# Optimization experiments

Hardware: AMD Instinct MI355X
Metric: run time of the kernel (lower is better)

Reference implementation:

```python
import jax, jax.numpy as jnp
import numpy as np

_P = ((0, 0), (1, 1), (1, 1), (0, 0))  # pad 1 on H and W (mypadding with sigma_fill=0)

_SHAPES = [
    ("e1a", (3, 3, 3, 64)), ("e1b", (3, 3, 64, 64)),
    ("e2a", (3, 3, 64, 128)), ("e2b", (3, 3, 128, 128)),
    ("ba", (3, 3, 128, 256)), ("bb", (3, 3, 256, 256)),
    ("d2u", (3, 3, 256, 128)), ("d2a", (3, 3, 256, 128)), ("d2b", (3, 3, 128, 128)),
    ("d1u", (3, 3, 128, 64)), ("d1a", (3, 3, 128, 64)), ("d1b", (3, 3, 64, 64)),
    ("fin", (1, 1, 64, 2)),
]


def _conv(x, w):
    return jax.lax.conv_general_dilated(x, w, (1, 1), 'VALID',
                                        dimension_numbers=('NHWC', 'HWIO', 'NHWC'))


def _conv_input(x, w_mu, w_sig):
    # mu = conv(x, w_mu); sigma = (sum over patch of x^2) * softplus(w_sigma)
    mu = _conv(x, w_mu)
    ws = jax.nn.softplus(w_sig)
    k, _, cin, _ = w_mu.shape
    ones = jnp.ones((k, k, cin, 1), x.dtype)
    s = _conv(x * x, ones) * ws
    return mu, s


def _conv_inter(x, s_in, w_mu, w_sig):
    # sigma = x^2 (x) w_sig + s_in (x) w_mu^2 + s_in (x) w_sig   (patch-sum form)
    mu = _conv(x, w_mu)
    ws = jax.nn.softplus(w_sig)
    k, _, cin, _ = w_mu.shape
    ones = jnp.ones((k, k, cin, 1), x.dtype)
    s = (_conv(x * x, ones) + _conv(s_in, ones)) * ws + _conv(s_in, w_mu * w_mu)
    return mu, s


def _relu(mu, s):
    g = (mu > 0).astype(mu.dtype)  # grad of ReLU; g^2 == g
    return jnp.maximum(mu, 0.0), g * s


def _pool(mu, s):
    # 2x2/stride-2 max pool with argmax; sigma gathered at argmax locations
    B, H, W, C = mu.shape

    def win(t):
        return t.reshape(B, H // 2, 2, W // 2, 2, C).transpose(0, 1, 3, 5, 2, 4).reshape(
            B, H // 2, W // 2, C, 4)

    mw, sw = win(mu), win(s)
    idx = jnp.argmax(mw, axis=-1)[..., None]
    mu_out = jnp.take_along_axis(mw, idx, axis=-1)[..., 0]
    s_out = jnp.take_along_axis(sw, idx, axis=-1)[..., 0]
    return mu_out, s_out


def _unpool(x):
    # zero-insertion: out[b, 2i+1, 2j+1, c] = x[b, i, j, c]; shape [B, 2H+1, 2W+1, C]
    B, H, W, C = x.shape
    out = jnp.zeros((B, 2 * H + 1, 2 * W + 1, C), x.dtype)
    return out.at[:, 1::2, 1::2, :].set(x)


def _crop(enc, dec):
    dh = (enc.shape[1] - dec.shape[1]) // 2
    dw = (enc.shape[2] - dec.shape[2]) // 2
    return enc[:, dh:dh + dec.shape[1], dw:dw + dec.shape[2], :]


def _softmax_prop(mu, s):
    B, H, W, C = mu.shape
    m = mu.reshape(B, -1, C)
    sg = s.reshape(B, -1, C)
    p = jax.nn.softmax(m, axis=-1)
    eye = jnp.eye(C, dtype=p.dtype)
    grad = p[..., :, None] * eye - p[..., :, None] * p[..., None, :]  # diag(p) - p p^T
    s_out = jnp.einsum('bnij,bnj->bni', grad * grad, sg)
    return p, s_out


def setup_inputs() -> dict:
    key = jax.random.key(0)
    out = {"x": jax.random.normal(jax.random.fold_in(key, 999), (4, 128, 128, 3), dtype=jnp.float32)}
    for i, (name, sh) in enumerate(_SHAPES):
        out[f"w_mu_{name}"] = 0.1 * jax.random.normal(jax.random.fold_in(key, i), sh, dtype=jnp.float32)
        out[f"w_sig_{name}"] = jax.random.uniform(jax.random.fold_in(key, 100 + i), (sh[-1],),
                                                  minval=-12.0, maxval=-4.6, dtype=jnp.float32)
    return out


def reference(x, w_mu_e1a, w_sig_e1a, w_mu_e1b, w_sig_e1b, w_mu_e2a, w_sig_e2a,
              w_mu_e2b, w_sig_e2b, w_mu_ba, w_sig_ba, w_mu_bb, w_sig_bb,
              w_mu_d2u, w_sig_d2u, w_mu_d2a, w_sig_d2a, w_mu_d2b, w_sig_d2b,
              w_mu_d1u, w_sig_d1u, w_mu_d1a, w_sig_d1a, w_mu_d1b, w_sig_d1b,
              w_mu_fin, w_sig_fin):
    # encoder level 1
    mu, s = _conv_input(jnp.pad(x, _P), w_mu_e1a, w_sig_e1a)
    mu, s = _relu(mu, s)
    mu, s = _conv_inter(jnp.pad(mu, _P), jnp.pad(s, _P), w_mu_e1b, w_sig_e1b)
    muE1, sE1 = _relu(mu, s)                       # [4,128,128,64]
    mu, s = _pool(muE1, sE1)                       # [4,64,64,64]
    # encoder level 2
    mu, s = _conv_inter(jnp.pad(mu, _P), jnp.pad(s, _P), w_mu_e2a, w_sig_e2a)
    mu, s = _relu(mu, s)
    mu, s = _conv_inter(jnp.pad(mu, _P), jnp.pad(s, _P), w_mu_e2b, w_sig_e2b)
    muE2, sE2 = _relu(mu, s)                       # [4,64,64,128]
    mu, s = _pool(muE2, sE2)                       # [4,32,32,128]
    # bottleneck
    mu, s = _conv_inter(jnp.pad(mu, _P), jnp.pad(s, _P), w_mu_ba, w_sig_ba)
    mu, s = _relu(mu, s)
    mu, s = _conv_inter(jnp.pad(mu, _P), jnp.pad(s, _P), w_mu_bb, w_sig_bb)
    mu, s = _relu(mu, s)                           # [4,32,32,256]
    # decoder level 2
    mu, s = _unpool(mu), _unpool(s)                # [4,65,65,256]
    mu, s = _conv_inter(mu, s, w_mu_d2u, w_sig_d2u)  # VALID -> [4,63,63,128]
    mu, s = _relu(mu, s)
    mu = jnp.concatenate([mu, _crop(muE2, mu)], axis=-1)
    s = jnp.concatenate([s, _crop(sE2, s)], axis=-1)  # [4,63,63,256]
    mu, s = _conv_inter(jnp.pad(mu, _P), jnp.pad(s, _P), w_mu_d2a, w_sig_d2a)
    mu, s = _relu(mu, s)
    mu, s = _conv_inter(jnp.pad(mu, _P), jnp.pad(s, _P), w_mu_d2b, w_sig_d2b)
    mu, s = _relu(mu, s)                           # [4,63,63,128]
    # decoder level 1
    mu, s = _unpool(mu), _unpool(s)                # [4,127,127,128]
    mu, s = _conv_inter(mu, s, w_mu_d1u, w_sig_d1u)  # VALID -> [4,125,125,64]
    mu, s = _relu(mu, s)
    mu = jnp.concatenate([mu, _crop(muE1, mu)], axis=-1)
    s = jnp.concatenate([s, _crop(sE1, s)], axis=-1)  # [4,125,125,128]
    mu, s = _conv_inter(jnp.pad(mu, _P), jnp.pad(s, _P), w_mu_d1a, w_sig_d1a)
    mu, s = _relu(mu, s)
    mu, s = _conv_inter(jnp.pad(mu, _P), jnp.pad(s, _P), w_mu_d1b, w_sig_d1b)
    mu, s = _relu(mu, s)
    # 1x1 classification conv + pixel-wise softmax density propagation
    mu, s = _conv_inter(mu, s, w_mu_fin, w_sig_fin)  # [4,125,125,2]
    return _softmax_prop(mu, s)                      # ([4,15625,2], [4,15625,2])
```

## Files before the change

kernel.cpp:

```cpp
#include <hip/hip_runtime.h>
#include <math.h>


typedef __attribute__((ext_vector_type(8))) short short8;
typedef __attribute__((ext_vector_type(4))) float floatx4;

__device__ __forceinline__ float softplus_f(float x) { return log1pf(expf(x)); }

__device__ __forceinline__ unsigned short f2bf(float x) {
    unsigned int u = __float_as_uint(x);
    u = (u + 0x7FFF + ((u >> 16) & 1)) >> 16;
    return (unsigned short)u;
}
__device__ __forceinline__ float bfval(unsigned short h) {
    return __uint_as_float((unsigned int)h << 16);
}

struct WMeta {
    const float* w[12];
    const float* wsig[12];
    int woff_[12];
    int spoff_[12];
    int cin_[12];
    int cout_[12];
    int nlayers;
    int totalW;
    int totalSp;
};

__global__ void wprep_all_kernel(WMeta m,
                                 unsigned short* __restrict__ wTh,
                                 unsigned short* __restrict__ wTl,
                                 unsigned short* __restrict__ wTsq,
                                 float* __restrict__ spb)
{
    int idx = blockIdx.x * blockDim.x + threadIdx.x;
    if (idx < m.totalW) {
        int l = 0;
        while (l + 1 < m.nlayers && idx >= m.woff_[l + 1]) l++;
        int local = idx - m.woff_[l];
        int Cin = m.cin_[l], Cout = m.cout_[l];
        int per = Cin * Cout;
        int tap = local / per;
        int rem = local - tap * per;
        int co = rem / Cin;
        int ci = rem - co * Cin;
        float v = m.w[l][(size_t)(tap * Cin + ci) * Cout + co];
        unsigned short hh = f2bf(v);
        wTh[idx] = hh;
        wTl[idx] = f2bf(v - bfval(hh));
        wTsq[idx] = f2bf(v * v);
    } else if (idx < m.totalW + m.totalSp) {
        int j = idx - m.totalW;
        int l = 0;
        while (l + 1 < m.nlayers && j >= m.spoff_[l + 1]) l++;
        spb[j] = softplus_f(m.wsig[l][j - m.spoff_[l]]);
    }
}

__global__ void __launch_bounds__(256)
fused_layer_kernel(const unsigned short* __restrict__ m1h, const unsigned short* __restrict__ m1l,
                   const unsigned short* __restrict__ s1h, const unsigned short* __restrict__ s1l,
                   const unsigned short* __restrict__ m2h, const unsigned short* __restrict__ m2l,
                   const unsigned short* __restrict__ s2h, const unsigned short* __restrict__ s2l,
                   const unsigned short* __restrict__ wTh, const unsigned short* __restrict__ wTl,
                   const unsigned short* __restrict__ wTsq,
                   const float* __restrict__ spv_,
                   float* __restrict__ oMf, float* __restrict__ oSf,
                   unsigned short* __restrict__ oMh, unsigned short* __restrict__ oMl,
                   unsigned short* __restrict__ oSh, unsigned short* __restrict__ oSl,
                   int B_, int H, int W, int Hin, int Win, int unpoolMode,
                   int Cin1, int Cin2,
                   int H2, int W2, int dh, int dw, int Cout)
{
    __shared__ unsigned short ldsB[3 * 2304];
    const int tid = threadIdx.x;
    const int lane = tid & 63;
    const int wave = tid >> 6;
    const int total = B_ * H * W;
    const int Cin = Cin1 + Cin2;
    const int ntiles = Cout >> 6;
    const int nPixBlk = (total + 63) >> 6;
    const int nReal = nPixBlk * ntiles;
    const int chunk = (int)gridDim.x >> 3;
    int gid = ((int)blockIdx.x & 7) * chunk + ((int)blockIdx.x >> 3);
    if (gid >= nReal) return;
    const int coTile = gid % ntiles;
    const int pixBlk = gid / ntiles;
    const int pixBase = pixBlk * 64 + wave * 16;
    const int coBase = coTile * 64;
    const int row = lane & 15;
    const int quad = lane >> 4;

    const unsigned short* wsel0; const unsigned short* wsel1; const unsigned short* wsel2;
    int tofs0, tofs1, tofs2;
    int ldso0, ldso1, ldso2;
    {
        int u = tid * 3;
        int arr = u >> 8, rem = u & 255, co = rem >> 2, part = rem & 3;
        wsel0 = (arr == 0) ? wTh : (arr == 1) ? wTl : wTsq;
        tofs0 = co * Cin + part * 8;
        ldso0 = arr * 2304 + co * 36 + part * 8;
        u++;
        arr = u >> 8; rem = u & 255; co = rem >> 2; part = rem & 3;
        wsel1 = (arr == 0) ? wTh : (arr == 1) ? wTl : wTsq;
        tofs1 = co * Cin + part * 8;
        ldso1 = arr * 2304 + co * 36 + part * 8;
        u++;
        arr = u >> 8; rem = u & 255; co = rem >> 2; part = rem & 3;
        wsel2 = (arr == 0) ? wTh : (arr == 1) ? wTl : wTsq;
        tofs2 = co * Cin + part * 8;
        ldso2 = arr * 2304 + co * 36 + part * 8;
    }

    int P = pixBase + row;
    bool pv = P < total;
    int Pc = pv ? P : 0;
    int pb = Pc / (H * W);
    int r0i = Pc - pb * (H * W);
    int ph = r0i / W;
    int pw = r0i - ph * W;

    floatx4 accM[4], accS[4];
#pragma unroll
    for (int i = 0; i < 4; i++) {
        accM[i] = (floatx4){0.f, 0.f, 0.f, 0.f};
        accS[i] = (floatx4){0.f, 0.f, 0.f, 0.f};
    }
    const short8 zero8 = {0, 0, 0, 0, 0, 0, 0, 0};
    float qacc = 0.f;

    const size_t tapstep = (size_t)Cout * Cin;
    size_t tapbase = (size_t)coBase * Cin;

    uint4 pf0 = *(const uint4*)(wsel0 + tapbase + tofs0);
    uint4 pf1 = *(const uint4*)(wsel1 + tapbase + tofs1);
    uint4 pf2 = *(const uint4*)(wsel2 + tapbase + tofs2);

    for (int tap = 0; tap < 9; tap++, tapbase += tapstep) {
        int kh = tap / 3, kw = tap - kh * 3;
        int ih, iw;
        bool tv;
        if (unpoolMode) {
            int uh = ph + kh, uw = pw + kw;
            tv = pv && (uh & 1) && (uw & 1);
            ih = (uh - 1) >> 1;
            iw = (uw - 1) >> 1;
        } else {
            ih = ph + kh - 1;
            iw = pw + kw - 1;
            tv = pv && ((unsigned)ih < (unsigned)Hin) && ((unsigned)iw < (unsigned)Win);
        }
        if (!tv) { ih = 0; iw = 0; }
        const int nsrc = (Cin2 > 0) ? 2 : 1;
        for (int src = 0; src < nsrc; src++) {
            const int csrc = src ? Cin2 : Cin1;
            const int cofs = src ? Cin1 : 0;
            const unsigned short* aMhp = src ? m2h : m1h;
            const unsigned short* aMlp = src ? m2l : m1l;
            const unsigned short* aShp = src ? s2h : s1h;
            const unsigned short* aSlp = src ? s2l : s1l;
            size_t ab;
            if (src) ab = ((size_t)(pb * H2 + ih + dh) * W2 + (iw + dw)) * (size_t)Cin2 + quad * 8;
            else     ab = ((size_t)(pb * Hin + ih) * Win + iw) * (size_t)Cin1 + quad * 8;
            for (int kb = 0; kb < csrc; kb += 32) {
                __syncthreads();
                *(uint4*)(&ldsB[ldso0]) = pf0;
                *(uint4*)(&ldsB[ldso1]) = pf1;
                *(uint4*)(&ldsB[ldso2]) = pf2;
                __syncthreads();
                short8 aMh = zero8, aMl = zero8, aSh = zero8, aSl = zero8;
                if (tv) {
                    aMh = *(const short8*)(aMhp + ab + kb);
                    aMl = *(const short8*)(aMlp + ab + kb);
                    aSh = *(const short8*)(aShp + ab + kb);
                    aSl = *(const short8*)(aSlp + ab + kb);
#pragma unroll
                    for (int e = 0; e < 8; e++) {
                        float m = bfval((unsigned short)aMh[e]) + bfval((unsigned short)aMl[e]);
                        qacc += m * m
                              + bfval((unsigned short)aSh[e]) + bfval((unsigned short)aSl[e]);
                    }
                }
                {
                    int ncol = cofs + kb + 32;
                    size_t nbase;
                    bool hn;
                    if (ncol < Cin) { nbase = tapbase + ncol; hn = true; }
                    else            { nbase = tapbase + tapstep; hn = (tap < 8); }
                    if (hn) {
                        pf0 = *(const uint4*)(wsel0 + nbase + tofs0);
                        pf1 = *(const uint4*)(wsel1 + nbase + tofs1);
                        pf2 = *(const uint4*)(wsel2 + nbase + tofs2);
                    }
                }
#pragma unroll
                for (int nt = 0; nt < 4; nt++) {
                    int lo = (nt * 16 + row) * 36 + quad * 8;
                    short8 bh = *(const short8*)(&ldsB[lo]);
                    short8 bl = *(const short8*)(&ldsB[2304 + lo]);
                    short8 bq = *(const short8*)(&ldsB[4608 + lo]);
                    accM[nt] = __builtin_amdgcn_mfma_f32_16x16x32_bf16(aMh, bh, accM[nt], 0, 0, 0);
                    accM[nt] = __builtin_amdgcn_mfma_f32_16x16x32_bf16(aMl, bh, accM[nt], 0, 0, 0);
                    accM[nt] = __builtin_amdgcn_mfma_f32_16x16x32_bf16(aMh, bl, accM[nt], 0, 0, 0);
                    accM[nt] = __builtin_amdgcn_mfma_f32_16x16x32_bf16(aMl, bl, accM[nt], 0, 0, 0);
                    accS[nt] = __builtin_amdgcn_mfma_f32_16x16x32_bf16(aSh, bq, accS[nt], 0, 0, 0);
                    accS[nt] = __builtin_amdgcn_mfma_f32_16x16x32_bf16(aSl, bq, accS[nt], 0, 0, 0);
                }
            }
        }
    }

    qacc += __shfl_xor(qacc, 16);
    qacc += __shfl_xor(qacc, 32);

#pragma unroll
    for (int nt = 0; nt < 4; nt++) {
        int co = coBase + nt * 16 + row;
        float spv = spv_[co];
        floatx4 am = accM[nt];
        floatx4 as = accS[nt];
#pragma unroll
        for (int r = 0; r < 4; r++) {
            int P2 = pixBase + quad * 4 + r;
            float qv = __shfl(qacc, quad * 4 + r);
            if (P2 < total) {
                size_t o = (size_t)P2 * Cout + co;
                float mu = am[r];
                float s = qv * spv + as[r];
                if (!(mu > 0.f)) { mu = 0.f; s = 0.f; }
                if (oMf) oMf[o] = mu;
                if (oSf) oSf[o] = s;
                if (oMh) {
                    unsigned short mh = f2bf(mu);
                    oMh[o] = mh;
                    oMl[o] = f2bf(mu - bfval(mh));
                    unsigned short sh = f2bf(s);
                    oSh[o] = sh;
                    oSl[o] = f2bf(s - bfval(sh));
                }
            }
        }
    }
}

__global__ void conv_input_relu_kernel(const float* __restrict__ x,
                                       const float* __restrict__ w_mu,
                                       const float* __restrict__ w_sig,
                                       unsigned short* __restrict__ m_h,
                                       unsigned short* __restrict__ m_l,
                                       unsigned short* __restrict__ s_h,
                                       unsigned short* __restrict__ s_l,
                                       int B_, int H, int W, int Cin, int Cout)
{
    int co = threadIdx.x;
    int pix = blockIdx.x * blockDim.y + threadIdx.y;
    int total = B_ * H * W;
    if (pix >= total) return;
    int b = pix / (H * W);
    int rem = pix % (H * W);
    int h = rem / W, w = rem % W;

    float mu = 0.f, q = 0.f;
    for (int kh = 0; kh < 3; kh++) {
        int ih = h + kh - 1;
        if (ih < 0 || ih >= H) continue;
        for (int kw = 0; kw < 3; kw++) {
            int iw = w + kw - 1;
            if (iw < 0 || iw >= W) continue;
            const float* xp = x + ((size_t)(b * H + ih) * W + iw) * Cin;
            const float* wp = w_mu + (size_t)((kh * 3 + kw) * Cin) * Cout + co;
            for (int ci = 0; ci < Cin; ci++) {
                float xv = xp[ci];
                mu += xv * wp[(size_t)ci * Cout];
                q += xv * xv;
            }
        }
    }
    float s = q * softplus_f(w_sig[co]);
    if (!(mu > 0.f)) { mu = 0.f; s = 0.f; }
    size_t oidx = (size_t)pix * Cout + co;
    unsigned short mh = f2bf(mu);
    m_h[oidx] = mh;
    m_l[oidx] = f2bf(mu - bfval(mh));
    unsigned short sh = f2bf(s);
    s_h[oidx] = sh;
    s_l[oidx] = f2bf(s - bfval(sh));
}

__global__ void pool_kernel(const float* __restrict__ mu_in,
                            const unsigned short* __restrict__ s_h,
                            const unsigned short* __restrict__ s_l,
                            unsigned short* __restrict__ pm_h,
                            unsigned short* __restrict__ pm_l,
                            unsigned short* __restrict__ ps_h,
                            unsigned short* __restrict__ ps_l,
                            int B_, int H, int W, int C)
{
    int Ho = H / 2, Wo = W / 2;
    size_t total = (size_t)B_ * Ho * Wo * C;
    size_t idx = (size_t)blockIdx.x * blockDim.x + threadIdx.x;
    if (idx >= total) return;
    int c = idx % C;
    size_t t = idx / C;
    int w = t % Wo; t /= Wo;
    int h = t % Ho;
    int b = t / Ho;
    size_t i0 = ((size_t)(b * H + 2 * h) * W + 2 * w) * C + c;
    size_t rowStride = (size_t)W * C;
    float m00 = mu_in[i0], m01 = mu_in[i0 + C];
    float m10 = mu_in[i0 + rowStride], m11 = mu_in[i0 + rowStride + C];
    int best = 0; float bm = m00;
    if (m01 > bm) { bm = m01; best = 1; }
    if (m10 > bm) { bm = m10; best = 2; }
    if (m11 > bm) { bm = m11; best = 3; }
    size_t off = (size_t)(best >> 1) * rowStride + (size_t)(best & 1) * C;
    unsigned short mh = f2bf(bm);
    pm_h[idx] = mh;
    pm_l[idx] = f2bf(bm - bfval(mh));
    ps_h[idx] = s_h[i0 + off];
    ps_l[idx] = s_l[i0 + off];
}

__global__ void final_kernel(const float* __restrict__ mu_in,
                             const float* __restrict__ s_in,
                             const float* __restrict__ w_mu,
                             const float* __restrict__ w_sig,
                             float* __restrict__ out,
                             int B_, int H, int W, int Cin)
{
    int pix = blockIdx.x * blockDim.x + threadIdx.x;
    int total = B_ * H * W;
    if (pix >= total) return;
    const float* mp = mu_in + (size_t)pix * Cin;
    const float* sp = s_in + (size_t)pix * Cin;
    float mu0 = 0.f, mu1 = 0.f, s0a = 0.f, s1a = 0.f, q = 0.f;
    for (int ci = 0; ci < Cin; ci += 4) {
        float4 m = *(const float4*)(mp + ci);
        float4 s = *(const float4*)(sp + ci);
        float4 wa = *(const float4*)(w_mu + ci * 2);
        float4 wb = *(const float4*)(w_mu + ci * 2 + 4);
        mu0 += m.x * wa.x + m.y * wa.z + m.z * wb.x + m.w * wb.z;
        mu1 += m.x * wa.y + m.y * wa.w + m.z * wb.y + m.w * wb.w;
        s0a += s.x * (wa.x * wa.x) + s.y * (wa.z * wa.z) + s.z * (wb.x * wb.x) + s.w * (wb.z * wb.z);
        s1a += s.x * (wa.y * wa.y) + s.y * (wa.w * wa.w) + s.z * (wb.y * wb.y) + s.w * (wb.w * wb.w);
        q += m.x * m.x + s.x + m.y * m.y + s.y + m.z * m.z + s.z + m.w * m.w + s.w;
    }
    float s0 = q * softplus_f(w_sig[0]) + s0a;
    float s1 = q * softplus_f(w_sig[1]) + s1a;
    float mx = fmaxf(mu0, mu1);
    float e0 = expf(mu0 - mx), e1 = expf(mu1 - mx);
    float inv = 1.f / (e0 + e1);
    float p0 = e0 * inv, p1 = e1 * inv;
    float g00 = p0 - p0 * p0, g01 = -p0 * p1;
    float g10 = -p1 * p0,     g11 = p1 - p1 * p1;
    float so0 = g00 * g00 * s0 + g01 * g01 * s1;
    float so1 = g10 * g10 * s0 + g11 * g11 * s1;
    out[(size_t)pix * 2]     = p0;
    out[(size_t)pix * 2 + 1] = p1;
    size_t off = (size_t)total * 2;
    out[off + (size_t)pix * 2]     = so0;
    out[off + (size_t)pix * 2 + 1] = so1;
}


extern "C" void kernel_launch(void* const* d_in, const int* in_sizes, int n_in,
                              void* d_out, int out_size, void* d_ws, size_t ws_size,
                              hipStream_t stream)
{
    const float* x = (const float*)d_in[0];
    enum { E1A, E1B, E2A, E2B, BA, BB, D2U, D2A, D2B, D1U, D1A, D1B, FIN, NW };
    const float* wmu[NW];
    const float* wsig[NW];
    for (int i = 0; i < NW; i++) {
        wmu[i]  = (const float*)d_in[1 + 2 * i];
        wsig[i] = (const float*)d_in[2 + 2 * i];
    }

    const int B_ = 4;
    float* ws = (float*)d_ws;
    float* M0  = ws;
    float* SF  = ws + 4194304;
    float* spb = ws + 8519680;
    unsigned short* us = (unsigned short*)(ws + 8521728);
    const size_t NB = 4194304;
    unsigned short* aMh = us;
    unsigned short* aMl = us + NB;
    unsigned short* aSh = us + 2 * NB;
    unsigned short* aSl = us + 3 * NB;
    unsigned short* bMh = us + 4 * NB;
    unsigned short* bMl = us + 5 * NB;
    unsigned short* bSh = us + 6 * NB;
    unsigned short* bSl = us + 7 * NB;
    unsigned short* e1Mh = us + 8 * NB;
    unsigned short* e1Ml = us + 9 * NB;
    unsigned short* e1Sh = us + 10 * NB;
    unsigned short* e1Sl = us + 11 * NB;
    unsigned short* e2Mh = us + 12 * NB;
    unsigned short* e2Ml = e2Mh + 2097152;
    unsigned short* e2Sh = e2Ml + 2097152;
    unsigned short* e2Sl = e2Sh + 2097152;
    unsigned short* wTh  = e2Sl + 2097152;
    unsigned short* wTl  = wTh + 2064384;
    unsigned short* wTsq = wTl + 2064384;

    const int mlay[11]  = {E1B, E2A, E2B, BA, BB, D2U, D2A, D2B, D1U, D1A, D1B};
    const int mcin[11]  = {64, 64, 128, 128, 256, 256, 256, 128, 128, 128, 64};
    const int mcout[11] = {64, 128, 128, 256, 256, 128, 128, 128, 64, 64, 64};
    size_t woff[NW]; int spoff[NW];
    {
        WMeta meta;
        int wo = 0, so = 0;
        for (int i = 0; i < 11; i++) {
            int l = mlay[i];
            woff[l] = (size_t)wo; spoff[l] = so;
            meta.w[i] = wmu[l];
            meta.wsig[i] = wsig[l];
            meta.woff_[i] = wo;
            meta.spoff_[i] = so;
            meta.cin_[i] = mcin[i];
            meta.cout_[i] = mcout[i];
            wo += 9 * mcin[i] * mcout[i];
            so += mcout[i];
        }
        meta.nlayers = 11;
        meta.totalW = wo;
        meta.totalSp = so;
        int n = wo + so;
        wprep_all_kernel<<<dim3((n + 255) / 256), dim3(256), 0, stream>>>(
            meta, wTh, wTl, wTsq, spb);
    }

    auto flayer = [&](const unsigned short* i_mh, const unsigned short* i_ml,
                      const unsigned short* i_sh, const unsigned short* i_sl, int ci1,
                      const unsigned short* k_mh, const unsigned short* k_ml,
                      const unsigned short* k_sh, const unsigned short* k_sl,
                      int ci2, int h2, int w2, int dh, int dw,
                      int H, int W, int widx, int cout,
                      float* oMf, float* oSf,
                      unsigned short* oMh, unsigned short* oMl,
                      unsigned short* oSh, unsigned short* oSl) {
        int total = B_ * H * W;
        int nReal = ((total + 63) / 64) * (cout / 64);
        int G = ((nReal + 7) / 8) * 8;
        fused_layer_kernel<<<dim3(G), dim3(256), 0, stream>>>(
            i_mh, i_ml, i_sh, i_sl, k_mh, k_ml, k_sh, k_sl,
            wTh + woff[widx], wTl + woff[widx], wTsq + woff[widx], spb + spoff[widx],
            oMf, oSf, oMh, oMl, oSh, oSl,
            B_, H, W, H, W, 0, ci1, ci2, h2, w2, dh, dw, cout);
    };

    auto ulayer = [&](const unsigned short* i_mh, const unsigned short* i_ml,
                      const unsigned short* i_sh, const unsigned short* i_sl, int ci,
                      int Hin, int Win, int widx, int cout,
                      unsigned short* oMh, unsigned short* oMl,
                      unsigned short* oSh, unsigned short* oSl) {
        int Hout = 2 * Hin - 1, Wout = 2 * Win - 1;
        int total = B_ * Hout * Wout;
        int nReal = ((total + 63) / 64) * (cout / 64);
        int G = ((nReal + 7) / 8) * 8;
        fused_layer_kernel<<<dim3(G), dim3(256), 0, stream>>>(
            i_mh, i_ml, i_sh, i_sl, nullptr, nullptr, nullptr, nullptr,
            wTh + woff[widx], wTl + woff[widx], wTsq + woff[widx], spb + spoff[widx],
            nullptr, nullptr, oMh, oMl, oSh, oSl,
            B_, Hout, Wout, Hin, Win, 1, ci, 0, 0, 0, 0, 0, cout);
    };

    {
        int totalPix = B_ * 128 * 128;
        conv_input_relu_kernel<<<dim3((totalPix + 3) / 4), dim3(64, 4), 0, stream>>>(
            x, wmu[E1A], wsig[E1A], aMh, aMl, aSh, aSl, B_, 128, 128, 3, 64);
    }
    flayer(aMh, aMl, aSh, aSl, 64, nullptr, nullptr, nullptr, nullptr, 0, 0, 0, 0, 0,
           128, 128, E1B, 64, M0, nullptr, e1Mh, e1Ml, e1Sh, e1Sl);
    {
        size_t total = (size_t)B_ * 64 * 64 * 64;
        pool_kernel<<<dim3((total + 255) / 256), dim3(256), 0, stream>>>(
            M0, e1Sh, e1Sl, bMh, bMl, bSh, bSl, B_, 128, 128, 64);
    }
    flayer(bMh, bMl, bSh, bSl, 64, nullptr, nullptr, nullptr, nullptr, 0, 0, 0, 0, 0,
           64, 64, E2A, 128, nullptr, nullptr, aMh, aMl, aSh, aSl);
    flayer(aMh, aMl, aSh, aSl, 128, nullptr, nullptr, nullptr, nullptr, 0, 0, 0, 0, 0,
           64, 64, E2B, 128, M0, nullptr, e2Mh, e2Ml, e2Sh, e2Sl);
    {
        size_t total = (size_t)B_ * 32 * 32 * 128;
        pool_kernel<<<dim3((total + 255) / 256), dim3(256), 0, stream>>>(
            M0, e2Sh, e2Sl, bMh, bMl, bSh, bSl, B_, 64, 64, 128);
    }
    flayer(bMh, bMl, bSh, bSl, 128, nullptr, nullptr, nullptr, nullptr, 0, 0, 0, 0, 0,
           32, 32, BA, 256, nullptr, nullptr, aMh, aMl, aSh, aSl);
    flayer(aMh, aMl, aSh, aSl, 256, nullptr, nullptr, nullptr, nullptr, 0, 0, 0, 0, 0,
           32, 32, BB, 256, nullptr, nullptr, bMh, bMl, bSh, bSl);
    ulayer(bMh, bMl, bSh, bSl, 256, 32, 32, D2U, 128, aMh, aMl, aSh, aSl);
    flayer(aMh, aMl, aSh, aSl, 128, e2Mh, e2Ml, e2Sh, e2Sl, 128, 64, 64, 0, 0,
           63, 63, D2A, 128, nullptr, nullptr, bMh, bMl, bSh, bSl);
    flayer(bMh, bMl, bSh, bSl, 128, nullptr, nullptr, nullptr, nullptr, 0, 0, 0, 0, 0,
           63, 63, D2B, 128, nullptr, nullptr, aMh, aMl, aSh, aSl);
    ulayer(aMh, aMl, aSh, aSl, 128, 63, 63, D1U, 64, bMh, bMl, bSh, bSl);
    flayer(bMh, bMl, bSh, bSl, 64, e1Mh, e1Ml, e1Sh, e1Sl, 64, 128, 128, 1, 1,
           125, 125, D1A, 64, nullptr, nullptr, aMh, aMl, aSh, aSl);
    flayer(aMh, aMl, aSh, aSl, 64, nullptr, nullptr, nullptr, nullptr, 0, 0, 0, 0, 0,
           125, 125, D1B, 64, M0, SF, nullptr, nullptr, nullptr, nullptr);
    {
        int totalPix = B_ * 125 * 125;
        final_kernel<<<dim3((totalPix + 63) / 64), dim3(64), 0, stream>>>(
            M0, SF, wmu[FIN], wsig[FIN], (float*)d_out, B_, 125, 125, 64);
    }
}
```

Measured before the change: 974.2 us.

## Add parity-class unpool conv kernel that skips zero-inserted taps

Adds a dedicated kernel for the transposed-convolution (unpool + 3x3 VALID conv) layers. Output pixels are split into four parity classes, and each class iterates only over the taps that hit real (non-zero) input values: 1, 2 or 4 taps instead of 9. This removes the MFMA work and loads that the generic fused kernel spent on inserted zeros. The cost is a separate code path with more index arithmetic and scattered output stores, plus per-class tiles that can be partially empty.

```diff
diff --git a/kernel.cpp b/kernel.cpp
--- a/kernel.cpp
+++ b/kernel.cpp
@@ -244,6 +244,170 @@
     }
 }
 
+__global__ void __launch_bounds__(256)
+fused_unpool_kernel(const unsigned short* __restrict__ m1h, const unsigned short* __restrict__ m1l,
+                    const unsigned short* __restrict__ s1h, const unsigned short* __restrict__ s1l,
+                    const unsigned short* __restrict__ wTh, const unsigned short* __restrict__ wTl,
+                    const unsigned short* __restrict__ wTsq,
+                    const float* __restrict__ spv_,
+                    unsigned short* __restrict__ oMh, unsigned short* __restrict__ oMl,
+                    unsigned short* __restrict__ oSh, unsigned short* __restrict__ oSl,
+                    int B_, int H, int W, int Hin, int Win,
+                    int Cin, int Cout)
+{
+    __shared__ unsigned short ldsB[3 * 2304];
+    const int tid = threadIdx.x;
+    const int lane = tid & 63;
+    const int wave = tid >> 6;
+    const int He = (H + 1) >> 1, Hd = H >> 1;
+    const int We = (W + 1) >> 1, Wd = W >> 1;
+    const int n00 = B_ * He * We, n01 = B_ * He * Wd;
+    const int n10 = B_ * Hd * We, n11 = B_ * Hd * Wd;
+    const int nb00 = (n00 + 63) >> 6, nb01 = (n01 + 63) >> 6;
+    const int nb10 = (n10 + 63) >> 6, nb11 = (n11 + 63) >> 6;
+    const int ntiles = Cout >> 6;
+    const int nReal = (nb00 + nb01 + nb10 + nb11) * ntiles;
+    const int chunk = (int)gridDim.x >> 3;
+    int gid = ((int)blockIdx.x & 7) * chunk + ((int)blockIdx.x >> 3);
+    if (gid >= nReal) return;
+    const int coTile = gid % ntiles;
+    int bid = gid / ntiles;
+    int hpar, wpar, classN, Wc, Hc;
+    if (bid < nb00)                    { hpar = 0; wpar = 0; classN = n00; Hc = He; Wc = We; }
+    else if (bid < nb00 + nb01)        { bid -= nb00; hpar = 0; wpar = 1; classN = n01; Hc = He; Wc = Wd; }
+    else if (bid < nb00 + nb01 + nb10) { bid -= nb00 + nb01; hpar = 1; wpar = 0; classN = n10; Hc = Hd; Wc = We; }
+    else                               { bid -= nb00 + nb01 + nb10; hpar = 1; wpar = 1; classN = n11; Hc = Hd; Wc = Wd; }
+    const int coBase = coTile * 64;
+    const int row = lane & 15;
+    const int quad = lane >> 4;
+    const int pixBase = bid * 64 + wave * 16;
+
+    const unsigned short* wsel0; const unsigned short* wsel1; const unsigned short* wsel2;
+    int tofs0, tofs1, tofs2, ldso0, ldso1, ldso2;
+    {
+        int u = tid * 3;
+        int arr = u >> 8, rem = u & 255, co = rem >> 2, part = rem & 3;
+        wsel0 = (arr == 0) ? wTh : (arr == 1) ? wTl : wTsq;
+        tofs0 = co * Cin + part * 8;
+        ldso0 = arr * 2304 + co * 36 + part * 8;
+        u++;
+        arr = u >> 8; rem = u & 255; co = rem >> 2; part = rem & 3;
+        wsel1 = (arr == 0) ? wTh : (arr == 1) ? wTl : wTsq;
+        tofs1 = co * Cin + part * 8;
+        ldso1 = arr * 2304 + co * 36 + part * 8;
+        u++;
+        arr = u >> 8; rem = u & 255; co = rem >> 2; part = rem & 3;
+        wsel2 = (arr == 0) ? wTh : (arr == 1) ? wTl : wTsq;
+        tofs2 = co * Cin + part * 8;
+        ldso2 = arr * 2304 + co * 36 + part * 8;
+    }
+
+    int gp = pixBase + row;
+    bool pv = gp < classN;
+    int gpc = pv ? gp : 0;
+    int hw = Hc * Wc;
+    int img = gpc / hw;
+    int rr = gpc - img * hw;
+    int hh = ((rr / Wc) << 1) + hpar;
+    int ww = ((rr - (rr / Wc) * Wc) << 1) + wpar;
+
+    floatx4 accM[4], accS[4];
+#pragma unroll
+    for (int i = 0; i < 4; i++) {
+        accM[i] = (floatx4){0.f, 0.f, 0.f, 0.f};
+        accS[i] = (floatx4){0.f, 0.f, 0.f, 0.f};
+    }
+    const short8 zero8 = {0, 0, 0, 0, 0, 0, 0, 0};
+    float qacc = 0.f;
+
+    const size_t tapstep = (size_t)Cout * Cin;
+    const size_t cobase_off = (size_t)coBase * Cin;
+
+#pragma unroll
+    for (int a = 0; a < 2; a++) {
+        if (a == 1 && hpar == 0) break;
+        int kh = hpar ? (a << 1) : 1;
+#pragma unroll
+        for (int b = 0; b < 2; b++) {
+            if (b == 1 && wpar == 0) break;
+            int kw = wpar ? (b << 1) : 1;
+            int tap = kh * 3 + kw;
+            size_t tapbase = (size_t)tap * tapstep + cobase_off;
+            int ih = (hh + kh - 1) >> 1;
+            int iw = (ww + kw - 1) >> 1;
+            size_t ab = ((size_t)(img * Hin + ih) * Win + iw) * (size_t)Cin + quad * 8;
+            for (int kb = 0; kb < Cin; kb += 32) {
+                __syncthreads();
+                uint4 w0 = *(const uint4*)(wsel0 + tapbase + kb + tofs0);
+                uint4 w1 = *(const uint4*)(wsel1 + tapbase + kb + tofs1);
+                uint4 w2 = *(const uint4*)(wsel2 + tapbase + kb + tofs2);
+                *(uint4*)(&ldsB[ldso0]) = w0;
+                *(uint4*)(&ldsB[ldso1]) = w1;
+                *(uint4*)(&ldsB[ldso2]) = w2;
+                __syncthreads();
+                short8 aMh = zero8, aMl = zero8, aSh = zero8, aSl = zero8;
+                if (pv) {
+                    aMh = *(const short8*)(m1h + ab + kb);
+                    aMl = *(const short8*)(m1l + ab + kb);
+                    aSh = *(const short8*)(s1h + ab + kb);
+                    aSl = *(const short8*)(s1l + ab + kb);
+#pragma unroll
+                    for (int e = 0; e < 8; e++) {
+                        float m = bfval((unsigned short)aMh[e]) + bfval((unsigned short)aMl[e]);
+                        qacc += m * m
+                              + bfval((unsigned short)aSh[e]) + bfval((unsigned short)aSl[e]);
+                    }
+                }
+#pragma unroll
+                for (int nt = 0; nt < 4; nt++) {
+                    int lo = (nt * 16 + row) * 36 + quad * 8;
+                    short8 bh = *(const short8*)(&ldsB[lo]);
+                    short8 bl = *(const short8*)(&ldsB[2304 + lo]);
+                    short8 bq = *(const short8*)(&ldsB[4608 + lo]);
+                    accM[nt] = __builtin_amdgcn_mfma_f32_16x16x32_bf16(aMh, bh, accM[nt], 0, 0, 0);
+                    accM[nt] = __builtin_amdgcn_mfma_f32_16x16x32_bf16(aMl, bh, accM[nt], 0, 0, 0);
+                    accM[nt] = __builtin_amdgcn_mfma_f32_16x16x32_bf16(aMh, bl, accM[nt], 0, 0, 0);
+                    accM[nt] = __builtin_amdgcn_mfma_f32_16x16x32_bf16(aMl, bl, accM[nt], 0, 0, 0);
+                    accS[nt] = __builtin_amdgcn_mfma_f32_16x16x32_bf16(aSh, bq, accS[nt], 0, 0, 0);
+                    accS[nt] = __builtin_amdgcn_mfma_f32_16x16x32_bf16(aSl, bq, accS[nt], 0, 0, 0);
+                }
+            }
+        }
+    }
+
+    qacc += __shfl_xor(qacc, 16);
+    qacc += __shfl_xor(qacc, 32);
+
+#pragma unroll
+    for (int nt = 0; nt < 4; nt++) {
+        int co = coBase + nt * 16 + row;
+        float spv = spv_[co];
+        floatx4 am = accM[nt];
+        floatx4 as = accS[nt];
+#pragma unroll
+        for (int r = 0; r < 4; r++) {
+            int gp2 = pixBase + quad * 4 + r;
+            float qv = __shfl(qacc, quad * 4 + r);
+            if (gp2 < classN) {
+                int img2 = gp2 / hw;
+                int rr2 = gp2 - img2 * hw;
+                int h2 = ((rr2 / Wc) << 1) + hpar;
+                int w2 = ((rr2 - (rr2 / Wc) * Wc) << 1) + wpar;
+                size_t o = ((size_t)(img2 * H + h2) * W + w2) * Cout + co;
+                float mu = am[r];
+                float s = qv * spv + as[r];
+                if (!(mu > 0.f)) { mu = 0.f; s = 0.f; }
+                unsigned short mh = f2bf(mu);
+                oMh[o] = mh;
+                oMl[o] = f2bf(mu - bfval(mh));
+                unsigned short sh = f2bf(s);
+                oSh[o] = sh;
+                oSl[o] = f2bf(s - bfval(sh));
+            }
+        }
+    }
+}
+
 __global__ void conv_input_relu_kernel(const float* __restrict__ x,
                                        const float* __restrict__ w_mu,
                                        const float* __restrict__ w_sig,
@@ -456,14 +620,17 @@
                       unsigned short* oMh, unsigned short* oMl,
                       unsigned short* oSh, unsigned short* oSl) {
         int Hout = 2 * Hin - 1, Wout = 2 * Win - 1;
-        int total = B_ * Hout * Wout;
-        int nReal = ((total + 63) / 64) * (cout / 64);
+        int He = (Hout + 1) / 2, Hd = Hout / 2;
+        int We = (Wout + 1) / 2, Wd = Wout / 2;
+        int nb = (B_ * He * We + 63) / 64 + (B_ * He * Wd + 63) / 64
+               + (B_ * Hd * We + 63) / 64 + (B_ * Hd * Wd + 63) / 64;
+        int nReal = nb * (cout / 64);
         int G = ((nReal + 7) / 8) * 8;
-        fused_layer_kernel<<<dim3(G), dim3(256), 0, stream>>>(
-            i_mh, i_ml, i_sh, i_sl, nullptr, nullptr, nullptr, nullptr,
+        fused_unpool_kernel<<<dim3(G), dim3(256), 0, stream>>>(
+            i_mh, i_ml, i_sh, i_sl,
             wTh + woff[widx], wTl + woff[widx], wTsq + woff[widx], spb + spoff[widx],
-            nullptr, nullptr, oMh, oMl, oSh, oSl,
-            B_, Hout, Wout, Hin, Win, 1, ci, 0, 0, 0, 0, 0, cout);
+            oMh, oMl, oSh, oSl,
+            B_, Hout, Wout, Hin, Win, ci, cout);
     };
 
     {
```

New measurement: 967.7 us, median of 2. No clear change (-0.7%).
